# Optimization experiments

Measured on AMD Instinct MI355X. Metric: run time of the kernel, lower is better.

Reference implementation:

```python
import jax, jax.numpy as jnp
import numpy as np

N_E = 200000   # number of entities
N_T = 1000000  # number of KB triples
N_R = 200      # number of relations
N_W2V = 300    # question embedding dim
B = 64         # batch size


def _one_step(x, r, subj, rel, obj):
    # torch.sparse.mm(M_subj, x.T)      -> gather: x[:, subj]  (B, N_T)
    # torch.sparse.mm(M_rel.T, r.T)     -> gather: r[:, rel]   (B, N_T)
    # torch.sparse.mm(M_obj.T, x_t*r_t) -> scatter-add over obj ids
    m = x[:, subj] * r[:, rel]                                   # (B, N_T)
    x_new = jax.ops.segment_sum(m.T, obj, num_segments=N_E).T    # (B, N_E)
    return x_new


def setup_inputs() -> dict:
    key = jax.random.key(0)
    ks = jax.random.split(key, 11)
    x = jax.random.uniform(ks[0], (B, N_E), dtype=jnp.float32)
    q = jax.random.normal(ks[1], (B, N_W2V), dtype=jnp.float32)
    subj = jax.random.randint(ks[2], (N_T,), 0, N_E, dtype=jnp.int32)
    rel = jax.random.randint(ks[3], (N_T,), 0, N_R, dtype=jnp.int32)
    obj = jax.random.randint(ks[4], (N_T,), 0, N_E, dtype=jnp.int32)
    s = 1.0 / np.sqrt(N_W2V)  # nn.Linear default init scale
    W1 = jax.random.uniform(ks[5], (N_W2V, N_R), minval=-s, maxval=s, dtype=jnp.float32)
    b1 = jax.random.uniform(ks[6], (N_R,), minval=-s, maxval=s, dtype=jnp.float32)
    W2 = jax.random.uniform(ks[7], (N_W2V, N_R), minval=-s, maxval=s, dtype=jnp.float32)
    b2 = jax.random.uniform(ks[8], (N_R,), minval=-s, maxval=s, dtype=jnp.float32)
    W3 = jax.random.uniform(ks[9], (N_W2V, N_R), minval=-s, maxval=s, dtype=jnp.float32)
    b3 = jax.random.uniform(ks[10], (N_R,), minval=-s, maxval=s, dtype=jnp.float32)
    return {"x": x, "q": q, "W1": W1, "b1": b1, "W2": W2, "b2": b2,
            "W3": W3, "b3": b3, "subj": subj, "rel": rel, "obj": obj,
            "n_hop": 3}


def reference(x, q, W1, b1, W2, b2, W3, b3, subj, rel, obj, n_hop):
    layers = [(W1, b1), (W2, b2), (W3, b3)]
    for W, b in layers[:n_hop]:
        r = q @ W + b              # dense_i(q): (B, N_R)
        x = _one_step(x, r, subj, rel, obj)
    return x
```

## Files before the change

kernel.cpp:

```cpp
#include <hip/hip_runtime.h>
#include <hip/hip_fp16.h>

#define WAVE 64
#define NXCD 8
#define NRMAX 200
#define RSTRIDE 17
#define HOP_TPB 1024
#define HOP_BLOCKS 512
#define CSR_BLOCKS 2048
#define CSR_TPB 256
#define CAP 16
#define OVF_CAP 32768

typedef int v4i __attribute__((ext_vector_type(4)));

__global__ void compute_r_kernel(const float* __restrict__ q,
                                 const float* __restrict__ W1, const float* __restrict__ b1,
                                 const float* __restrict__ W2, const float* __restrict__ b2,
                                 const float* __restrict__ W3, const float* __restrict__ b3,
                                 float* __restrict__ rT, int N_R, int N_W2V) {
    int lane = threadIdx.x & 63;
    int wv   = threadIdx.x >> 6;
    int b    = blockIdx.y * 4 + wv;
    int it   = blockIdx.x * 64 + lane;
    if (it >= 3 * N_R) return;
    int l = it / N_R;
    int j = it - l * N_R;
    const float* W  = (l == 0) ? W1 : (l == 1) ? W2 : W3;
    const float* bv = (l == 0) ? b1 : (l == 1) ? b2 : b3;
    const float* qrow = q + (size_t)b * N_W2V;
    float a0 = 0.f, a1 = 0.f, a2 = 0.f, a3 = 0.f;
    int k = 0;
    for (; k + 4 <= N_W2V; k += 4) {
        a0 = fmaf(qrow[k + 0], W[(size_t)(k + 0) * N_R + j], a0);
        a1 = fmaf(qrow[k + 1], W[(size_t)(k + 1) * N_R + j], a1);
        a2 = fmaf(qrow[k + 2], W[(size_t)(k + 2) * N_R + j], a2);
        a3 = fmaf(qrow[k + 3], W[(size_t)(k + 3) * N_R + j], a3);
    }
    for (; k < N_W2V; ++k)
        a0 = fmaf(qrow[k], W[(size_t)k * N_R + j], a0);
    rT[(size_t)it * WAVE + b] = bv[j] + ((a0 + a1) + (a2 + a3));
}

__global__ void transpose_in_f16_kernel(const float* __restrict__ in, __half2* __restrict__ out, int N_E) {
    __shared__ float tile[64][65];
    int e0 = blockIdx.x * 64;
    int li = threadIdx.x & 63;
    int lo = threadIdx.x >> 6;
    #pragma unroll
    for (int k = 0; k < 16; ++k) {
        int b = lo + 4 * k;
        int e = e0 + li;
        tile[b][li] = (e < N_E) ? in[(size_t)b * N_E + e] : 0.0f;
    }
    __syncthreads();
    #pragma unroll
    for (int k = 0; k < 8; ++k) {
        int idx = k * 256 + threadIdx.x;
        int ei  = idx >> 5;
        int j   = idx & 31;
        int e   = e0 + ei;
        if (e < N_E)
            out[(size_t)e * 32 + j] = __floats2half2_rn(tile[2 * j][ei], tile[2 * j + 1][ei]);
    }
}


__global__ void scatter_direct_kernel(const int* __restrict__ subj, const int* __restrict__ rel,
                                      const int* __restrict__ obj,
                                      int* __restrict__ cnt, unsigned* __restrict__ slots,
                                      int* __restrict__ novf, int* __restrict__ ovf_obj,
                                      unsigned* __restrict__ ovf_pk, int nT, int nE) {
    int grp = blockIdx.x & (NXCD - 1);
    int sh  = (nE + NXCD - 1) / NXCD;
    int lo  = grp * sh;
    int hi  = min(nE, lo + sh);
    int tid    = (blockIdx.x >> 3) * blockDim.x + threadIdx.x;
    int stride = (gridDim.x >> 3) * blockDim.x;
    int nT4 = nT >> 2;
    const v4i* obj4 = (const v4i*)obj;
    for (int t = tid; t < nT4; t += stride) {
        v4i o = __builtin_nontemporal_load(obj4 + t);
        int base = t * 4;
        #pragma unroll
        for (int u = 0; u < 4; ++u) {
            int oo = o[u];
            if (oo >= lo && oo < hi) {
                unsigned s_ = (unsigned)__builtin_nontemporal_load(subj + base + u);
                unsigned r_ = (unsigned)__builtin_nontemporal_load(rel  + base + u);
                unsigned pk = s_ | (r_ << 18);
                int slot = atomicAdd(&cnt[oo], 1);
                if (slot < CAP) slots[(size_t)oo * CAP + slot] = pk;
                else {
                    int oi = atomicAdd(novf, 1);
                    if (oi < OVF_CAP) { ovf_obj[oi] = oo; ovf_pk[oi] = pk; }
                }
            }
        }
    }
    for (int t = nT4 * 4 + tid; t < nT; t += stride) {
        int oo = obj[t];
        if (oo >= lo && oo < hi) {
            unsigned pk = (unsigned)subj[t] | ((unsigned)rel[t] << 18);
            int slot = atomicAdd(&cnt[oo], 1);
            if (slot < CAP) slots[(size_t)oo * CAP + slot] = pk;
            else {
                int oi = atomicAdd(novf, 1);
                if (oi < OVF_CAP) { ovf_obj[oi] = oo; ovf_pk[oi] = pk; }
            }
        }
    }
}


__device__ __forceinline__ float4 h4_to_f4(uint2 v) {
    float2 f0 = __half22float2(*(__half2*)&v.x);
    float2 f1 = __half22float2(*(__half2*)&v.y);
    return make_float4(f0.x, f0.y, f1.x, f1.y);
}

__device__ __forceinline__ uint2 pack_half4(float4 a) {
    __half2 h0 = __floats2half2_rn(a.x, a.y);
    __half2 h1 = __floats2half2_rn(a.z, a.w);
    uint2 v;
    v.x = *(unsigned*)&h0;
    v.y = *(unsigned*)&h1;
    return v;
}

__device__ __forceinline__ float4 hop_accum4(const uint2* __restrict__ xp,
                                             const float4* __restrict__ r_lds,
                                             const int* __restrict__ cnt,
                                             const unsigned* __restrict__ slots,
                                             int e, int g, int c, int nE) {
    float4 acc = make_float4(0.f, 0.f, 0.f, 0.f);
    int len = (e < nE) ? min(cnt[e], CAP) : 0;
    unsigned pv = (c < len) ? slots[(size_t)e * CAP + c] : 0u;
    int m = max(len, __shfl_xor(len, 16));
    m = max(m, __shfl_xor(m, 32));
    for (int j0 = 0; j0 < m; j0 += 8) {
        uint2 xv[8];
        unsigned pr[8];
        #pragma unroll
        for (int u = 0; u < 8; ++u) {
            int jj = max(min(j0 + u, len - 1), 0);
            unsigned p = __shfl(pv, (g << 4) + jj);
            pr[u] = p >> 18;
            xv[u] = xp[(size_t)(p & 0x3FFFFu) * 16 + c];
        }
        #pragma unroll
        for (int u = 0; u < 8; ++u) {
            if (j0 + u < len) {
                float4 rv = r_lds[pr[u] * RSTRIDE + c];
                float4 xf = h4_to_f4(xv[u]);
                acc.x = fmaf(xf.x, rv.x, acc.x);
                acc.y = fmaf(xf.y, rv.y, acc.y);
                acc.z = fmaf(xf.z, rv.z, acc.z);
                acc.w = fmaf(xf.w, rv.w, acc.w);
            }
        }
    }
    return acc;
}

__global__ __launch_bounds__(HOP_TPB, 8)
void hop_mid_kernel(const uint2* __restrict__ xp, const float4* __restrict__ rT4,
                    const int* __restrict__ cnt, const unsigned* __restrict__ slots,
                    uint2* __restrict__ yh, int nE, int nR) {
    __shared__ float4 r_lds[NRMAX * RSTRIDE];
    for (int i = threadIdx.x; i < nR * 16; i += HOP_TPB)
        r_lds[(i >> 4) * RSTRIDE + (i & 15)] = rT4[i];
    __syncthreads();
    int lane = threadIdx.x & 63;
    int g = lane >> 4, c = lane & 15;
    int wv = threadIdx.x >> 6;
    int nTiles = (nE + 63) >> 6;
    for (int t = blockIdx.x; t < nTiles; t += gridDim.x) {
        int e = t * 64 + wv * 4 + g;
        float4 acc = hop_accum4(xp, r_lds, cnt, slots, e, g, c, nE);
        if (e < nE) yh[(size_t)e * 16 + c] = pack_half4(acc);
    }
}

__global__ __launch_bounds__(HOP_TPB, 8)
void hop_out_kernel(const uint2* __restrict__ xp, const float4* __restrict__ rT4,
                    const int* __restrict__ cnt, const unsigned* __restrict__ slots,
                    float* __restrict__ out, int nE, int nR) {
    __shared__ float4 r_lds[NRMAX * RSTRIDE];
    __shared__ float tile[64][65];
    for (int i = threadIdx.x; i < nR * 16; i += HOP_TPB)
        r_lds[(i >> 4) * RSTRIDE + (i & 15)] = rT4[i];
    __syncthreads();
    int lane = threadIdx.x & 63;
    int g = lane >> 4, c = lane & 15;
    int wv = threadIdx.x >> 6;
    int nTiles = (nE + 63) >> 6;
    for (int t = blockIdx.x; t < nTiles; t += gridDim.x) {
        int e0 = t * 64;
        int ei = wv * 4 + g;
        float4 acc = hop_accum4(xp, r_lds, cnt, slots, e0 + ei, g, c, nE);
        tile[ei][4 * c + 0] = acc.x;
        tile[ei][4 * c + 1] = acc.y;
        tile[ei][4 * c + 2] = acc.z;
        tile[ei][4 * c + 3] = acc.w;
        __syncthreads();
        #pragma unroll
        for (int k = 0; k < 4; ++k) {
            int b = wv * 4 + k;
            int e = e0 + lane;
            if (e < nE) out[(size_t)b * nE + e] = tile[lane][b];
        }
        __syncthreads();
    }
}

__device__ __forceinline__ void atom_add_h2(unsigned* addr, float a, float b) {
    unsigned old = __atomic_load_n(addr, __ATOMIC_RELAXED), assumed;
    do {
        assumed = old;
        float2 f = __half22float2(*(__half2*)&assumed);
        __half2 nh = __floats2half2_rn(f.x + a, f.y + b);
        old = atomicCAS(addr, assumed, *(unsigned*)&nh);
    } while (old != assumed);
}

__global__ void ovf_mid_kernel(const uint2* __restrict__ xp, const float* __restrict__ rTl,
                               const int* __restrict__ novf, const int* __restrict__ ovf_obj,
                               const unsigned* __restrict__ ovf_pk, uint2* __restrict__ yh) {
    int n = min(*novf, OVF_CAP);
    int c = threadIdx.x & 15, grp = threadIdx.x >> 4;
    for (int i = blockIdx.x * 4 + grp; i < n; i += gridDim.x * 4) {
        int o = ovf_obj[i];
        unsigned p = ovf_pk[i];
        float4 xf = h4_to_f4(xp[(size_t)(p & 0x3FFFFu) * 16 + c]);
        const float* rr = rTl + (size_t)(p >> 18) * 64 + c * 4;
        unsigned* w = (unsigned*)&yh[(size_t)o * 16 + c];
        atom_add_h2(w,     xf.x * rr[0], xf.y * rr[1]);
        atom_add_h2(w + 1, xf.z * rr[2], xf.w * rr[3]);
    }
}

__global__ void ovf_out_kernel(const uint2* __restrict__ xp, const float* __restrict__ rTl,
                               const int* __restrict__ novf, const int* __restrict__ ovf_obj,
                               const unsigned* __restrict__ ovf_pk, float* __restrict__ out, int nE) {
    int n = min(*novf, OVF_CAP);
    int c = threadIdx.x & 15, grp = threadIdx.x >> 4;
    for (int i = blockIdx.x * 4 + grp; i < n; i += gridDim.x * 4) {
        int o = ovf_obj[i];
        unsigned p = ovf_pk[i];
        float4 xf = h4_to_f4(xp[(size_t)(p & 0x3FFFFu) * 16 + c]);
        const float* rr = rTl + (size_t)(p >> 18) * 64 + c * 4;
        atomicAdd(&out[(size_t)(4 * c + 0) * nE + o], xf.x * rr[0]);
        atomicAdd(&out[(size_t)(4 * c + 1) * nE + o], xf.y * rr[1]);
        atomicAdd(&out[(size_t)(4 * c + 2) * nE + o], xf.z * rr[2]);
        atomicAdd(&out[(size_t)(4 * c + 3) * nE + o], xf.w * rr[3]);
    }
}

extern "C" void kernel_launch(void* const* d_in, const int* in_sizes, int n_in,
                              void* d_out, int out_size, void* d_ws, size_t ws_size,
                              hipStream_t stream) {
    const float* x  = (const float*)d_in[0];
    const float* q  = (const float*)d_in[1];
    const float* W1 = (const float*)d_in[2];
    const float* b1 = (const float*)d_in[3];
    const float* W2 = (const float*)d_in[4];
    const float* b2 = (const float*)d_in[5];
    const float* W3 = (const float*)d_in[6];
    const float* b3 = (const float*)d_in[7];
    const int* subj = (const int*)d_in[8];
    const int* rel  = (const int*)d_in[9];
    const int* obj  = (const int*)d_in[10];

    const int B     = 64;
    const int N_E   = in_sizes[0] / B;
    const int N_W2V = in_sizes[1] / B;
    const int N_R   = in_sizes[3];
    const int N_T   = in_sizes[8];

    const size_t h16bytes = (size_t)N_E * B * sizeof(__half);

    int*      cnt     = (int*)d_ws;
    int*      novf    = cnt + N_E;
    int*      ovf_obj = novf + 4;
    unsigned* ovf_pk  = (unsigned*)(ovf_obj + OVF_CAP);
    unsigned* slots   = ovf_pk + OVF_CAP;
    char*     rT_raw  = (char*)(slots + (size_t)N_E * CAP);
    float*    rT      = (float*)(((uintptr_t)rT_raw + 15) & ~(uintptr_t)15);
    char*     X0      = (char*)(rT + (size_t)3 * N_R * B);
    size_t used = (size_t)(X0 - (char*)d_ws) + h16bytes;

    char* H1;
    if (ws_size >= used + h16bytes) {
        H1 = X0 + h16bytes;
        used += h16bytes;
    } else {
        H1 = (char*)d_out;
    }
    char* H2 = X0;

    {
        dim3 rgrid((3 * N_R + 63) / 64, B / 4);
        compute_r_kernel<<<rgrid, 256, 0, stream>>>(q, W1, b1, W2, b2, W3, b3, rT, N_R, N_W2V);
    }

    int tgrid = (N_E + 63) / 64;
    transpose_in_f16_kernel<<<tgrid, 256, 0, stream>>>(x, (__half2*)X0, N_E);

    hipMemsetAsync(cnt, 0, (size_t)(N_E + 4) * sizeof(int), stream);
    scatter_direct_kernel<<<CSR_BLOCKS, CSR_TPB, 0, stream>>>(
        subj, rel, obj, cnt, slots, novf, ovf_obj, ovf_pk, N_T, N_E);

    int nTiles  = (N_E + 63) / 64;
    int hblocks = nTiles < HOP_BLOCKS ? nTiles : HOP_BLOCKS;
    const float* rT1 = rT;
    const float* rT2 = rT + (size_t)1 * N_R * B;
    const float* rT3 = rT + (size_t)2 * N_R * B;

    hop_mid_kernel<<<hblocks, HOP_TPB, 0, stream>>>(
        (const uint2*)X0, (const float4*)rT1, cnt, slots, (uint2*)H1, N_E, N_R);
    ovf_mid_kernel<<<16, 64, 0, stream>>>(
        (const uint2*)X0, rT1, novf, ovf_obj, ovf_pk, (uint2*)H1);

    hop_mid_kernel<<<hblocks, HOP_TPB, 0, stream>>>(
        (const uint2*)H1, (const float4*)rT2, cnt, slots, (uint2*)H2, N_E, N_R);
    ovf_mid_kernel<<<16, 64, 0, stream>>>(
        (const uint2*)H1, rT2, novf, ovf_obj, ovf_pk, (uint2*)H2);

    hop_out_kernel<<<hblocks, HOP_TPB, 0, stream>>>(
        (const uint2*)H2, (const float4*)rT3, cnt, slots, (float*)d_out, N_E, N_R);
    ovf_out_kernel<<<16, 64, 0, stream>>>(
        (const uint2*)H2, rT3, novf, ovf_obj, ovf_pk, (float*)d_out, N_E);
}
```

Measured before the change: 365.4 us.

## Fuse prologue kernels and batch atomics in scatter loop

Merges the r-projection, the input transpose to fp16 and the counter memset into one prologue launch whose block ranges pick the job, removing two launches and a memset. In the scatter kernel, the four subj/rel loads and the four atomicAdds per vector are issued together so their latencies overlap, and the nontemporal load hints are dropped. The cost is more live registers in the scatter loop and slightly different caching of the index arrays.

```diff
diff --git a/kernel.cpp b/kernel.cpp
--- a/kernel.cpp
+++ b/kernel.cpp
@@ -14,54 +14,65 @@
 
 typedef int v4i __attribute__((ext_vector_type(4)));
 
-__global__ void compute_r_kernel(const float* __restrict__ q,
-                                 const float* __restrict__ W1, const float* __restrict__ b1,
-                                 const float* __restrict__ W2, const float* __restrict__ b2,
-                                 const float* __restrict__ W3, const float* __restrict__ b3,
-                                 float* __restrict__ rT, int N_R, int N_W2V) {
-    int lane = threadIdx.x & 63;
-    int wv   = threadIdx.x >> 6;
-    int b    = blockIdx.y * 4 + wv;
-    int it   = blockIdx.x * 64 + lane;
-    if (it >= 3 * N_R) return;
-    int l = it / N_R;
-    int j = it - l * N_R;
-    const float* W  = (l == 0) ? W1 : (l == 1) ? W2 : W3;
-    const float* bv = (l == 0) ? b1 : (l == 1) ? b2 : b3;
-    const float* qrow = q + (size_t)b * N_W2V;
-    float a0 = 0.f, a1 = 0.f, a2 = 0.f, a3 = 0.f;
-    int k = 0;
-    for (; k + 4 <= N_W2V; k += 4) {
-        a0 = fmaf(qrow[k + 0], W[(size_t)(k + 0) * N_R + j], a0);
-        a1 = fmaf(qrow[k + 1], W[(size_t)(k + 1) * N_R + j], a1);
-        a2 = fmaf(qrow[k + 2], W[(size_t)(k + 2) * N_R + j], a2);
-        a3 = fmaf(qrow[k + 3], W[(size_t)(k + 3) * N_R + j], a3);
-    }
-    for (; k < N_W2V; ++k)
-        a0 = fmaf(qrow[k], W[(size_t)k * N_R + j], a0);
-    rT[(size_t)it * WAVE + b] = bv[j] + ((a0 + a1) + (a2 + a3));
-}
-
-__global__ void transpose_in_f16_kernel(const float* __restrict__ in, __half2* __restrict__ out, int N_E) {
+
+__global__ void prologue_kernel(const float* __restrict__ x, const float* __restrict__ q,
+                                const float* __restrict__ W1, const float* __restrict__ b1,
+                                const float* __restrict__ W2, const float* __restrict__ b2,
+                                const float* __restrict__ W3, const float* __restrict__ b3,
+                                float* __restrict__ rT, __half2* __restrict__ xT,
+                                int* __restrict__ cnt, int N_E, int N_R, int N_W2V,
+                                int tgrid, int nrx, int rblocks, int zcount) {
     __shared__ float tile[64][65];
-    int e0 = blockIdx.x * 64;
-    int li = threadIdx.x & 63;
-    int lo = threadIdx.x >> 6;
-    #pragma unroll
-    for (int k = 0; k < 16; ++k) {
-        int b = lo + 4 * k;
-        int e = e0 + li;
-        tile[b][li] = (e < N_E) ? in[(size_t)b * N_E + e] : 0.0f;
-    }
-    __syncthreads();
-    #pragma unroll
-    for (int k = 0; k < 8; ++k) {
-        int idx = k * 256 + threadIdx.x;
-        int ei  = idx >> 5;
-        int j   = idx & 31;
-        int e   = e0 + ei;
-        if (e < N_E)
-            out[(size_t)e * 32 + j] = __floats2half2_rn(tile[2 * j][ei], tile[2 * j + 1][ei]);
+    int bid = blockIdx.x;
+    if (bid < tgrid) {
+        int e0 = bid * 64;
+        int li = threadIdx.x & 63;
+        int lo = threadIdx.x >> 6;
+        #pragma unroll
+        for (int k = 0; k < 16; ++k) {
+            int b = lo + 4 * k;
+            int e = e0 + li;
+            tile[b][li] = (e < N_E) ? x[(size_t)b * N_E + e] : 0.0f;
+        }
+        __syncthreads();
+        #pragma unroll
+        for (int k = 0; k < 8; ++k) {
+            int idx = k * 256 + threadIdx.x;
+            int ei  = idx >> 5;
+            int j   = idx & 31;
+            int e   = e0 + ei;
+            if (e < N_E)
+                xT[(size_t)e * 32 + j] = __floats2half2_rn(tile[2 * j][ei], tile[2 * j + 1][ei]);
+        }
+    } else if (bid < tgrid + rblocks) {
+        int rb = bid - tgrid;
+        int bx = rb % nrx;
+        int by = rb / nrx;
+        int lane = threadIdx.x & 63;
+        int wv   = threadIdx.x >> 6;
+        int b    = by * 4 + wv;
+        int it   = bx * 64 + lane;
+        if (it >= 3 * N_R) return;
+        int l = it / N_R;
+        int j = it - l * N_R;
+        const float* W  = (l == 0) ? W1 : (l == 1) ? W2 : W3;
+        const float* bv = (l == 0) ? b1 : (l == 1) ? b2 : b3;
+        const float* qrow = q + (size_t)b * N_W2V;
+        float a0 = 0.f, a1 = 0.f, a2 = 0.f, a3 = 0.f;
+        int k = 0;
+        for (; k + 4 <= N_W2V; k += 4) {
+            a0 = fmaf(qrow[k + 0], W[(size_t)(k + 0) * N_R + j], a0);
+            a1 = fmaf(qrow[k + 1], W[(size_t)(k + 1) * N_R + j], a1);
+            a2 = fmaf(qrow[k + 2], W[(size_t)(k + 2) * N_R + j], a2);
+            a3 = fmaf(qrow[k + 3], W[(size_t)(k + 3) * N_R + j], a3);
+        }
+        for (; k < N_W2V; ++k)
+            a0 = fmaf(qrow[k], W[(size_t)k * N_R + j], a0);
+        rT[(size_t)it * WAVE + b] = bv[j] + ((a0 + a1) + (a2 + a3));
+    } else {
+        int zb = bid - tgrid - rblocks;
+        int i4 = zb * 256 + threadIdx.x;
+        if (i4 < zcount) ((v4i*)cnt)[i4] = (v4i){0, 0, 0, 0};
     }
 }
 
@@ -80,20 +91,28 @@
     int nT4 = nT >> 2;
     const v4i* obj4 = (const v4i*)obj;
     for (int t = tid; t < nT4; t += stride) {
-        v4i o = __builtin_nontemporal_load(obj4 + t);
+        v4i o = obj4[t];
         int base = t * 4;
+        int  oo[4];
+        bool mk[4];
+        unsigned pk[4];
+        int  slot[4];
         #pragma unroll
         for (int u = 0; u < 4; ++u) {
-            int oo = o[u];
-            if (oo >= lo && oo < hi) {
-                unsigned s_ = (unsigned)__builtin_nontemporal_load(subj + base + u);
-                unsigned r_ = (unsigned)__builtin_nontemporal_load(rel  + base + u);
-                unsigned pk = s_ | (r_ << 18);
-                int slot = atomicAdd(&cnt[oo], 1);
-                if (slot < CAP) slots[(size_t)oo * CAP + slot] = pk;
+            oo[u] = o[u];
+            mk[u] = (oo[u] >= lo && oo[u] < hi);
+            pk[u] = mk[u] ? ((unsigned)subj[base + u] | ((unsigned)rel[base + u] << 18)) : 0u;
+        }
+        #pragma unroll
+        for (int u = 0; u < 4; ++u)
+            if (mk[u]) slot[u] = atomicAdd(&cnt[oo[u]], 1);
+        #pragma unroll
+        for (int u = 0; u < 4; ++u) {
+            if (mk[u]) {
+                if (slot[u] < CAP) slots[(size_t)oo[u] * CAP + slot[u]] = pk[u];
                 else {
                     int oi = atomicAdd(novf, 1);
-                    if (oi < OVF_CAP) { ovf_obj[oi] = oo; ovf_pk[oi] = pk; }
+                    if (oi < OVF_CAP) { ovf_obj[oi] = oo[u]; ovf_pk[oi] = pk[u]; }
                 }
             }
         }
@@ -299,20 +318,19 @@
     }
     char* H2 = X0;
 
-    {
-        dim3 rgrid((3 * N_R + 63) / 64, B / 4);
-        compute_r_kernel<<<rgrid, 256, 0, stream>>>(q, W1, b1, W2, b2, W3, b3, rT, N_R, N_W2V);
-    }
-
-    int tgrid = (N_E + 63) / 64;
-    transpose_in_f16_kernel<<<tgrid, 256, 0, stream>>>(x, (__half2*)X0, N_E);
-
-    hipMemsetAsync(cnt, 0, (size_t)(N_E + 4) * sizeof(int), stream);
+    int tgrid   = (N_E + 63) / 64;
+    int nrx     = (3 * N_R + 63) / 64;
+    int rblocks = nrx * (B / 4);
+    int zcount  = (N_E + 4) / 4;
+    int zblocks = (zcount + 255) / 256;
+    prologue_kernel<<<tgrid + rblocks + zblocks, 256, 0, stream>>>(
+        x, q, W1, b1, W2, b2, W3, b3, rT, (__half2*)X0, cnt,
+        N_E, N_R, N_W2V, tgrid, nrx, rblocks, zcount);
+
     scatter_direct_kernel<<<CSR_BLOCKS, CSR_TPB, 0, stream>>>(
         subj, rel, obj, cnt, slots, novf, ovf_obj, ovf_pk, N_T, N_E);
 
-    int nTiles  = (N_E + 63) / 64;
-    int hblocks = nTiles < HOP_BLOCKS ? nTiles : HOP_BLOCKS;
+    int hblocks = tgrid < HOP_BLOCKS ? tgrid : HOP_BLOCKS;
     const float* rT1 = rT;
     const float* rT2 = rT + (size_t)1 * N_R * B;
     const float* rT3 = rT + (size_t)2 * N_R * B;
```

Result: faster. 345.1 us (-5.6%).
